# Performance work log

Hardware: AMD Instinct MI355X
Metric: run time of the kernel (lower is better)

The kernel has to match this reference:

```python
import jax, jax.numpy as jnp
import numpy as np

B, S, D = 8, 1024, 1024
H, DH = 16, 64  # num_attention_heads, attention_head_size; H*DH == D


def setup_inputs() -> dict:
    key = jax.random.key(0)
    ks = jax.random.split(key, 6)
    scale = 0.02
    return {
        "hidden_states": jax.random.normal(ks[0], (B, S, D), jnp.float32),
        "right_hidden_states": jax.random.normal(ks[1], (B, S, D), jnp.float32),
        "attention_mask": jnp.ones((B, S, S), jnp.float32),
        "Wq": jax.random.normal(ks[2], (D, H * DH), jnp.float32) * scale,
        "bq": jnp.zeros((H * DH,), jnp.float32),
        "Wk": jax.random.normal(ks[3], (D, H * DH), jnp.float32) * scale,
        "bk": jnp.zeros((H * DH,), jnp.float32),
        "Wv": jax.random.normal(ks[4], (D, H * DH), jnp.float32) * scale,
        "bv": jnp.zeros((H * DH,), jnp.float32),
    }


def _split_heads(x, b):
    # (B, S, H*DH) -> (B, H, S, DH)
    return x.reshape(b, -1, H, DH).transpose(0, 2, 1, 3)


def reference(hidden_states, right_hidden_states, attention_mask, Wq, bq, Wk, bk, Wv, bv):
    b = hidden_states.shape[0]
    q = _split_heads(hidden_states @ Wq + bq, b)          # (B,H,Sq,DH)
    k = _split_heads(right_hidden_states @ Wk + bk, b)    # (B,H,Sk,DH)
    v = _split_heads(right_hidden_states @ Wv + bv, b)    # (B,H,Sk,DH)

    scores = jnp.einsum("bhqd,bhkd->bhqk", q, k) / jnp.sqrt(jnp.asarray(DH, q.dtype))
    scores = jnp.sum(scores, axis=1, keepdims=True)       # (B,1,Sq,Sk) head-summed

    ext = (1.0 - attention_mask[:, None, :, :].astype(scores.dtype)) * -1e9
    probs = jax.nn.softmax(scores + ext, axis=-1)         # (B,1,Sq,Sk)

    ctx = jnp.matmul(probs, v)                            # broadcast -> (B,H,Sq,DH)
    # Faithful to original: reshape WITHOUT transposing heads back.
    return ctx.reshape(b, -1, H * DH)                     # (B,Sq,H*DH)
```

## Files before the change

### kernel.cpp

```cpp
#include <hip/hip_runtime.h>
#include <stdint.h>

constexpr int S = 1024;
constexpr int D = 1024;
constexpr int NB = 8;

typedef __bf16 bf16x8 __attribute__((ext_vector_type(8)));
typedef float floatx4 __attribute__((ext_vector_type(4)));

#define AS1 __attribute__((address_space(1)))
#define AS3 __attribute__((address_space(3)))

__device__ __forceinline__ unsigned short f2bf(float f) {
  unsigned u = __builtin_bit_cast(unsigned, f);
  u += 0x7fffu + ((u >> 16) & 1u);
  return (unsigned short)(u >> 16);
}

__device__ __forceinline__ void gload16(const void* g, void* l) {
  __builtin_amdgcn_global_load_lds((const AS1 unsigned int*)g, (AS3 unsigned int*)l, 16, 0, 0);
}

__global__ __launch_bounds__(256) void prep_kernel(const float4* __restrict__ hs4,
                                                   const float4* __restrict__ rhs4,
                                                   ushort4* __restrict__ hsb4,
                                                   ushort4* __restrict__ rhsb4, int n4,
                                                   const float* __restrict__ Wq,
                                                   const float* __restrict__ Wk,
                                                   const float* __restrict__ Wv,
                                                   unsigned short* __restrict__ Wcat) {
  __shared__ float tile[32][33];
  const int bid = blockIdx.x;
  if (bid < 16384) {
    int i = bid * 256 + threadIdx.x;
    const float4* src;
    ushort4* dst;
    int j;
    if (i < n4) {
      src = hs4; dst = hsb4; j = i;
    } else {
      src = rhs4; dst = rhsb4; j = i - n4;
    }
    float4 v = src[j];
    ushort4 o;
    o.x = f2bf(v.x); o.y = f2bf(v.y); o.z = f2bf(v.z); o.w = f2bf(v.w);
    dst[j] = o;
  } else {
    const int t = bid - 16384;
    const int z = t >> 10;
    const int r = t & 1023;
    const float* W = (z == 0) ? Wq : (z == 1) ? Wk : Wv;
    unsigned short* Wt = Wcat + (long long)z * D * D;
    const int bx = (r & 31) * 32;
    const int by = (r >> 5) * 32;
    const int x = threadIdx.x & 31;
    const int y0 = threadIdx.x >> 5;
    for (int i = 0; i < 4; ++i) {
      int y = y0 + i * 8;
      tile[y][x] = W[(by + y) * D + bx + x];
    }
    __syncthreads();
    for (int i = 0; i < 4; ++i) {
      int y = y0 + i * 8;
      Wt[(long long)(bx + y) * D + by + x] = f2bf(tile[x][y]);
    }
  }
}


#define GEMM_STAGE_SETUP(Abase, lda_, Bbase, ldb_)                            \
  const int srow = tid >> 2;                                                  \
  const int scg = (((tid & 3) ^ ((srow >> 1) & 3)) * 8);                      \
  const unsigned short* aG0 = (Abase) + (long long)srow * (lda_) + scg;       \
  const unsigned short* aG1 = aG0 + (long long)64 * (lda_);                   \
  const unsigned short* bG0 = (Bbase) + (long long)srow * (ldb_) + scg;       \
  const unsigned short* bG1 = bG0 + (long long)64 * (ldb_);                   \
  unsigned short* aL0 = As + w * 512;                                         \
  unsigned short* aL1 = As + w * 512 + 2048;                                  \
  unsigned short* bL0 = Bs + w * 512;                                         \
  unsigned short* bL1 = Bs + w * 512 + 2048;

#define GEMM_KLOOP(Klen)                                                               \
  for (int k0 = 0; k0 < (Klen); k0 += 32) {                                            \
    gload16(aG0 + k0, aL0);                                                            \
    gload16(aG1 + k0, aL1);                                                            \
    gload16(bG0 + k0, bL0);                                                            \
    gload16(bG1 + k0, bL1);                                                            \
    __syncthreads();                                                                   \
    bf16x8 af[4], bfr[4];                                                              \
    for (int t = 0; t < 4; ++t) {                                                      \
      af[t] = *reinterpret_cast<const bf16x8*>(As + (wm + t * 16 + r15) * 32 + pq);    \
      bfr[t] = *reinterpret_cast<const bf16x8*>(Bs + (wn + t * 16 + r15) * 32 + pq);   \
    }                                                                                  \
    for (int mt = 0; mt < 4; ++mt)                                                     \
      for (int nt = 0; nt < 4; ++nt)                                                   \
        acc[mt][nt] =                                                                  \
            __builtin_amdgcn_mfma_f32_16x16x32_bf16(af[mt], bfr[nt], acc[mt][nt], 0, 0, 0); \
    __syncthreads();                                                                   \
  }

#define GEMM_COMMON_IDX                  \
  const int tid = threadIdx.x;           \
  const int lane = tid & 63;             \
  const int w = tid >> 6;                \
  const int r15 = lane & 15;             \
  const int quad = lane >> 4;            \
  const int pq = (quad ^ ((r15 >> 1) & 3)) * 8; \
  const int wm = (w >> 1) * 64;          \
  const int wn = (w & 1) * 64;

#define GEMM_ACC_INIT                    \
  floatx4 acc[4][4];                     \
  for (int i = 0; i < 4; ++i)            \
    for (int j = 0; j < 4; ++j) acc[i][j] = {0.f, 0.f, 0.f, 0.f};

__global__ __launch_bounds__(256, 3) void gemm_qkv_kernel(
    const unsigned short* __restrict__ hsb, const unsigned short* __restrict__ rhsb,
    const unsigned short* __restrict__ Wcat, unsigned short* __restrict__ Qm,
    unsigned short* __restrict__ Km, unsigned short* __restrict__ Vmt,
    const float* __restrict__ bq, const float* __restrict__ bk, const float* __restrict__ bv) {
  __shared__ __align__(16) unsigned short As[128 * 32];
  __shared__ __align__(16) unsigned short Bs[128 * 32];
  GEMM_COMMON_IDX
  const long long n0g = (long long)blockIdx.x * 128;
  const int seg = (int)(n0g >> 10);
  const long long m0 = (long long)blockIdx.y * 128;
  const unsigned short* A = ((seg == 0) ? hsb : rhsb) + m0 * D;
  const unsigned short* Bt = Wcat + n0g * D;
  const float* bias = (seg == 0) ? bq : (seg == 1) ? bk : bv;

  GEMM_STAGE_SETUP(A, D, Bt, D)
  GEMM_ACC_INIT
  GEMM_KLOOP(D)

  const long long nloc0 = n0g & 1023;
  for (int mt = 0; mt < 4; ++mt) {
    for (int nt = 0; nt < 4; ++nt) {
      const long long mrow = m0 + wm + mt * 16 + quad * 4;
      const long long nc = nloc0 + wn + nt * 16 + r15;
      const float bval = bias[nc];
      floatx4 v = acc[mt][nt];
      for (int e = 0; e < 4; ++e) {
        float val = v[e] + bval;
        long long m = mrow + e;
        if (seg == 0) {
          Qm[m * D + nc] = f2bf(val);
        } else if (seg == 1) {
          Km[m * D + nc] = f2bf(val);
        } else {
          Vmt[(m >> 10) * (long long)(S * D) + nc * S + (m & 1023)] = f2bf(val);
        }
      }
    }
  }
}

__global__ __launch_bounds__(256, 3) void gemm_scores_kernel(
    const unsigned short* __restrict__ Qm, const unsigned short* __restrict__ Km,
    const float* __restrict__ mask, unsigned short* __restrict__ E,
    float* __restrict__ rowsumP) {
  __shared__ __align__(16) unsigned short As[128 * 32];
  __shared__ __align__(16) unsigned short Bs[128 * 32];
  GEMM_COMMON_IDX
  const int bid = blockIdx.x;
  const int z = bid & 7;
  const int r = bid >> 3;
  const int by = r >> 3;
  const int bx = r & 7;
  const long long m0 = (long long)by * 128;
  const long long n0 = (long long)bx * 128;
  const unsigned short* A = Qm + (long long)z * S * D + m0 * D;
  const unsigned short* Bt = Km + (long long)z * S * D + n0 * D;

  GEMM_STAGE_SETUP(A, D, Bt, D)
  GEMM_ACC_INIT
  GEMM_KLOOP(D)

  const long long zE = (long long)z * S * 1024;
  float rowpart[4][4];
  for (int mt = 0; mt < 4; ++mt)
    for (int e = 0; e < 4; ++e) rowpart[mt][e] = 0.f;

  for (int mt = 0; mt < 4; ++mt) {
    for (int nt = 0; nt < 4; ++nt) {
      const long long mrow = m0 + wm + mt * 16 + quad * 4;
      const long long nc = n0 + wn + nt * 16 + r15;
      floatx4 v = acc[mt][nt];
      for (int e = 0; e < 4; ++e) {
        long long m = mrow + e;
        float mval = mask[zE + m * 1024 + nc];
        float sc = v[e] * 0.125f + (1.0f - mval) * -1e9f;
        float Ev = __expf(sc);
        E[zE + m * 1024 + nc] = f2bf(Ev);
        rowpart[mt][e] += Ev;
      }
    }
  }
  const int slot = (bx << 11) + ((wn >> 6) << 10);
  for (int mt = 0; mt < 4; ++mt) {
    for (int e = 0; e < 4; ++e) {
      float s = rowpart[mt][e];
      s += __shfl_xor(s, 1, 64);
      s += __shfl_xor(s, 2, 64);
      s += __shfl_xor(s, 4, 64);
      s += __shfl_xor(s, 8, 64);
      if (r15 == 0) {
        int mloc = (int)(m0 + wm + mt * 16 + quad * 4 + e);
        rowsumP[(z << 14) + slot + mloc] = s;
      }
    }
  }
}

__global__ __launch_bounds__(256, 3) void gemm_ctx_kernel(const unsigned short* __restrict__ E,
                                                          const unsigned short* __restrict__ Vmt,
                                                          const float* __restrict__ rowsumP,
                                                          float* __restrict__ out) {
  __shared__ __align__(16) unsigned short As[128 * 32];
  __shared__ __align__(16) unsigned short Bs[128 * 32];
  __shared__ float rsinv[128];
  GEMM_COMMON_IDX
  const int bid = blockIdx.x;
  const int z = bid & 7;
  const int r = bid >> 3;
  const int by = r >> 3;
  const int bx = r & 7;
  const long long m0 = (long long)by * 128;
  const long long n0 = (long long)bx * 128;
  const unsigned short* A = E + (long long)z * S * 1024 + m0 * 1024;
  const unsigned short* Bt = Vmt + (long long)z * S * D + n0 * D;

  if (tid < 128) {
    float s = 0.f;
    for (int t = 0; t < 16; ++t) s += rowsumP[(z << 14) + (t << 10) + (int)m0 + tid];
    rsinv[tid] = 1.0f / s;
  }

  GEMM_STAGE_SETUP(A, 1024, Bt, D)
  GEMM_ACC_INIT
  GEMM_KLOOP(1024)

  for (int mt = 0; mt < 4; ++mt) {
    for (int nt = 0; nt < 4; ++nt) {
      const int r0 = wm + mt * 16 + quad * 4;
      const long long ncol = n0 + wn + nt * 16 + r15;
      floatx4 v = acc[mt][nt];
      for (int e = 0; e < 4; ++e) {
        long long m = m0 + r0 + e;
        float val = v[e] * rsinv[r0 + e];
        out[(long long)z * S * D + (ncol >> 6) * (long long)(S * 64) + m * 64 + (ncol & 63)] =
            val;
      }
    }
  }
}

extern "C" void kernel_launch(void* const* d_in, const int* in_sizes, int n_in, void* d_out,
                              int out_size, void* d_ws, size_t ws_size, hipStream_t stream) {
  const float* hs = (const float*)d_in[0];
  const float* rhs = (const float*)d_in[1];
  const float* mask = (const float*)d_in[2];
  const float* Wq = (const float*)d_in[3];
  const float* bq = (const float*)d_in[4];
  const float* Wk = (const float*)d_in[5];
  const float* bk = (const float*)d_in[6];
  const float* Wv = (const float*)d_in[7];
  const float* bv = (const float*)d_in[8];
  float* out = (float*)d_out;
  char* ws = (char*)d_ws;
  const size_t MB = 1ull << 20;
  unsigned short* Wcat = (unsigned short*)(ws + 0 * MB);
  unsigned short* hsb = (unsigned short*)(ws + 6 * MB);
  unsigned short* rhsb = (unsigned short*)(ws + 22 * MB);
  unsigned short* Qm = (unsigned short*)(ws + 38 * MB);
  unsigned short* Km = (unsigned short*)(ws + 54 * MB);
  unsigned short* Vmt = (unsigned short*)(ws + 70 * MB);
  unsigned short* E = (unsigned short*)(ws + 6 * MB);
  float* rowsumP = (float*)(ws + 22 * MB);

  const int n4 = NB * S * D / 4;
  prep_kernel<<<16384 + 3072, 256, 0, stream>>>((const float4*)hs, (const float4*)rhs,
                                                (ushort4*)hsb, (ushort4*)rhsb, n4, Wq, Wk, Wv,
                                                Wcat);

  gemm_qkv_kernel<<<dim3(24, 64), 256, 0, stream>>>(hsb, rhsb, Wcat, Qm, Km, Vmt, bq, bk, bv);

  gemm_scores_kernel<<<dim3(512), 256, 0, stream>>>(Qm, Km, mask, E, rowsumP);

  gemm_ctx_kernel<<<dim3(512), 256, 0, stream>>>(E, Vmt, rowsumP, out);
}
```

Baseline: 295.0 us.

## Fold Wq·Wkᵀ into a single weight so the K projection GEMM is skipped

Head-summed scores equal hs·Wq·Wkᵀ·rhsᵀ plus bias terms. The change precomputes M = Wq·Wkᵀ/8 with a split-K GEMM, computes the bias cross terms as per-row vectors, then runs one GEMM hs·M and uses rhs directly as the key operand. This drops the separate Q and K projection GEMMs, leaving about two-thirds of the projection work. In exchange it adds a 1024³ weight-product GEMM and a cast pass, it skips the bias matvec when the bias vector is all zero, and it changes bf16 rounding because the precision of the product weight differs.

Result: slower. 309.7 us (+5.0%).

```diff
diff --git a/kernel.cpp b/kernel.cpp
--- a/kernel.cpp
+++ b/kernel.cpp
@@ -17,18 +17,22 @@
   return (unsigned short)(u >> 16);
 }
 
+__device__ __forceinline__ float bf2f(unsigned short x) {
+  unsigned u = ((unsigned)x) << 16;
+  return __builtin_bit_cast(float, u);
+}
+
 __device__ __forceinline__ void gload16(const void* g, void* l) {
   __builtin_amdgcn_global_load_lds((const AS1 unsigned int*)g, (AS3 unsigned int*)l, 16, 0, 0);
 }
 
-__global__ __launch_bounds__(256) void prep_kernel(const float4* __restrict__ hs4,
-                                                   const float4* __restrict__ rhs4,
-                                                   ushort4* __restrict__ hsb4,
-                                                   ushort4* __restrict__ rhsb4, int n4,
-                                                   const float* __restrict__ Wq,
-                                                   const float* __restrict__ Wk,
-                                                   const float* __restrict__ Wv,
-                                                   unsigned short* __restrict__ Wcat) {
+__global__ __launch_bounds__(256) void prep_kernel(
+    const float4* __restrict__ hs4, const float4* __restrict__ rhs4,
+    ushort4* __restrict__ hsb4, ushort4* __restrict__ rhsb4, int n4,
+    const float* __restrict__ Wq, const float* __restrict__ Wk, const float* __restrict__ Wv,
+    unsigned short* __restrict__ WvT, ushort4* __restrict__ Wqb4, ushort4* __restrict__ Wkb4,
+    const float* __restrict__ bq, const float* __restrict__ bk, float* __restrict__ u,
+    float* __restrict__ v, float* __restrict__ cbuf) {
   __shared__ float tile[32][33];
   const int bid = blockIdx.x;
   if (bid < 16384) {
@@ -41,29 +45,58 @@
     } else {
       src = rhs4; dst = rhsb4; j = i - n4;
     }
-    float4 v = src[j];
+    float4 w = src[j];
     ushort4 o;
-    o.x = f2bf(v.x); o.y = f2bf(v.y); o.z = f2bf(v.z); o.w = f2bf(v.w);
+    o.x = f2bf(w.x); o.y = f2bf(w.y); o.z = f2bf(w.z); o.w = f2bf(w.w);
     dst[j] = o;
-  } else {
-    const int t = bid - 16384;
-    const int z = t >> 10;
-    const int r = t & 1023;
-    const float* W = (z == 0) ? Wq : (z == 1) ? Wk : Wv;
-    unsigned short* Wt = Wcat + (long long)z * D * D;
+  } else if (bid < 18432) {
+    int j = (bid - 16384) * 256 + threadIdx.x;
+    const float4* src = (j < 262144) ? (const float4*)Wq : (const float4*)Wk;
+    ushort4* dst = (j < 262144) ? Wqb4 : Wkb4;
+    int jj = (j < 262144) ? j : j - 262144;
+    float4 w = src[jj];
+    ushort4 o;
+    o.x = f2bf(w.x); o.y = f2bf(w.y); o.z = f2bf(w.z); o.w = f2bf(w.w);
+    dst[jj] = o;
+  } else if (bid < 19456) {
+    const int r = bid - 18432;
     const int bx = (r & 31) * 32;
     const int by = (r >> 5) * 32;
     const int x = threadIdx.x & 31;
     const int y0 = threadIdx.x >> 5;
     for (int i = 0; i < 4; ++i) {
       int y = y0 + i * 8;
-      tile[y][x] = W[(by + y) * D + bx + x];
+      tile[y][x] = Wv[(by + y) * D + bx + x];
     }
     __syncthreads();
     for (int i = 0; i < 4; ++i) {
       int y = y0 + i * 8;
-      Wt[(long long)(bx + y) * D + by + x] = f2bf(tile[x][y]);
-    }
+      WvT[(long long)(bx + y) * D + by + x] = f2bf(tile[x][y]);
+    }
+  } else if (bid < 19460) {
+    const int d = (bid - 19456) * 256 + threadIdx.x;
+    const float* row = Wq + (long long)d * 1024;
+    float s = 0.f;
+    for (int c = 0; c < 1024; ++c) s += row[c] * bk[c];
+    u[d] = 0.125f * s;
+  } else if (bid < 19464) {
+    const int d = (bid - 19460) * 256 + threadIdx.x;
+    const float* row = Wk + (long long)d * 1024;
+    float s = 0.f;
+    for (int c = 0; c < 1024; ++c) s += row[c] * bq[c];
+    v[d] = 0.125f * s;
+  } else {
+    __shared__ float sh[256];
+    const int tid = threadIdx.x;
+    float s = 0.f;
+    for (int c = tid; c < 1024; c += 256) s += bq[c] * bk[c];
+    sh[tid] = s;
+    __syncthreads();
+    for (int o = 128; o; o >>= 1) {
+      if (tid < o) sh[tid] += sh[tid + o];
+      __syncthreads();
+    }
+    if (tid == 0) cbuf[0] = 0.125f * sh[0];
   }
 }
 
@@ -114,51 +147,119 @@
   for (int i = 0; i < 4; ++i)            \
     for (int j = 0; j < 4; ++j) acc[i][j] = {0.f, 0.f, 0.f, 0.f};
 
-__global__ __launch_bounds__(256, 3) void gemm_qkv_kernel(
+__global__ __launch_bounds__(256) void wprod_kernel(
+    const unsigned short* __restrict__ Wkb, const unsigned short* __restrict__ Wqb,
+    float* __restrict__ Mtf, const unsigned short* __restrict__ hsb,
+    const unsigned short* __restrict__ rhsb, const float* __restrict__ u,
+    const float* __restrict__ v, const float* __restrict__ cbuf, float* __restrict__ t2,
+    float* __restrict__ t3) {
+  __shared__ __align__(16) unsigned short As[128 * 32];
+  __shared__ __align__(16) unsigned short Bs[128 * 32];
+  const int bid = blockIdx.x;
+  if (bid < 256) {
+    GEMM_COMMON_IDX
+    const int tilei = bid & 63;
+    const int kc = bid >> 6;
+    const int bx = tilei & 7;
+    const int by = tilei >> 3;
+    const unsigned short* A = Wkb + (long long)by * 128 * D + kc * 256;
+    const unsigned short* Bt = Wqb + (long long)bx * 128 * D + kc * 256;
+    GEMM_STAGE_SETUP(A, D, Bt, D)
+    GEMM_ACC_INIT
+    GEMM_KLOOP(256)
+    float* dst = Mtf + ((long long)kc << 20);
+    for (int mt = 0; mt < 4; ++mt)
+      for (int nt = 0; nt < 4; ++nt) {
+        const int mrow = by * 128 + wm + mt * 16 + quad * 4;
+        const int nc = bx * 128 + wn + nt * 16 + r15;
+        floatx4 vv = acc[mt][nt];
+        for (int e = 0; e < 4; ++e) dst[(long long)(mrow + e) * 1024 + nc] = vv[e] * 0.125f;
+      }
+  } else {
+    const int tid = threadIdx.x;
+    const bool isT2 = bid < 288;
+    const int row = (isT2 ? (bid - 256) : (bid - 288)) * 256 + tid;
+    const float* vec = isT2 ? u : v;
+    const unsigned short* mat = isT2 ? hsb : rhsb;
+    float* out = isT2 ? t2 : t3;
+    __shared__ int nz;
+    if (tid == 0) nz = 0;
+    __syncthreads();
+    const float4* u4 = (const float4*)vec;
+    float4 uu = u4[tid];
+    if (uu.x != 0.f || uu.y != 0.f || uu.z != 0.f || uu.w != 0.f) nz = 1;
+    __syncthreads();
+    const float c2 = 0.5f * cbuf[0];
+    if (!nz) {
+      out[row] = c2;
+      return;
+    }
+    const ushort4* r4 = (const ushort4*)(mat + (long long)row * 1024);
+    float s = 0.f;
+    for (int c4 = 0; c4 < 256; ++c4) {
+      ushort4 h = r4[c4];
+      s += bf2f(h.x) * vec[c4 * 4 + 0] + bf2f(h.y) * vec[c4 * 4 + 1] +
+           bf2f(h.z) * vec[c4 * 4 + 2] + bf2f(h.w) * vec[c4 * 4 + 3];
+    }
+    out[row] = s + c2;
+  }
+}
+
+__global__ __launch_bounds__(256) void castM_kernel(const float4* __restrict__ Mtf4,
+                                                    ushort4* __restrict__ Mtb4) {
+  const int j = blockIdx.x * 256 + threadIdx.x;
+  float4 a = Mtf4[j];
+  float4 b = Mtf4[j + 262144];
+  float4 c = Mtf4[j + 524288];
+  float4 d = Mtf4[j + 786432];
+  ushort4 o;
+  o.x = f2bf(a.x + b.x + c.x + d.x);
+  o.y = f2bf(a.y + b.y + c.y + d.y);
+  o.z = f2bf(a.z + b.z + c.z + d.z);
+  o.w = f2bf(a.w + b.w + c.w + d.w);
+  Mtb4[j] = o;
+}
+
+__global__ __launch_bounds__(256) void gemm_fused_kernel(
     const unsigned short* __restrict__ hsb, const unsigned short* __restrict__ rhsb,
-    const unsigned short* __restrict__ Wcat, unsigned short* __restrict__ Qm,
-    unsigned short* __restrict__ Km, unsigned short* __restrict__ Vmt,
-    const float* __restrict__ bq, const float* __restrict__ bk, const float* __restrict__ bv) {
+    const unsigned short* __restrict__ Mtb, const unsigned short* __restrict__ WvT,
+    const float* __restrict__ bv, unsigned short* __restrict__ hsMb,
+    unsigned short* __restrict__ Vmt) {
   __shared__ __align__(16) unsigned short As[128 * 32];
   __shared__ __align__(16) unsigned short Bs[128 * 32];
   GEMM_COMMON_IDX
-  const long long n0g = (long long)blockIdx.x * 128;
-  const int seg = (int)(n0g >> 10);
+  const int seg = (int)(blockIdx.x >> 3);
+  const long long nloc = (blockIdx.x & 7) * 128;
   const long long m0 = (long long)blockIdx.y * 128;
   const unsigned short* A = ((seg == 0) ? hsb : rhsb) + m0 * D;
-  const unsigned short* Bt = Wcat + n0g * D;
-  const float* bias = (seg == 0) ? bq : (seg == 1) ? bk : bv;
+  const unsigned short* Bt = ((seg == 0) ? Mtb : WvT) + nloc * D;
 
   GEMM_STAGE_SETUP(A, D, Bt, D)
   GEMM_ACC_INIT
   GEMM_KLOOP(D)
 
-  const long long nloc0 = n0g & 1023;
   for (int mt = 0; mt < 4; ++mt) {
     for (int nt = 0; nt < 4; ++nt) {
       const long long mrow = m0 + wm + mt * 16 + quad * 4;
-      const long long nc = nloc0 + wn + nt * 16 + r15;
-      const float bval = bias[nc];
-      floatx4 v = acc[mt][nt];
-      for (int e = 0; e < 4; ++e) {
-        float val = v[e] + bval;
-        long long m = mrow + e;
-        if (seg == 0) {
-          Qm[m * D + nc] = f2bf(val);
-        } else if (seg == 1) {
-          Km[m * D + nc] = f2bf(val);
-        } else {
-          Vmt[(m >> 10) * (long long)(S * D) + nc * S + (m & 1023)] = f2bf(val);
+      const long long nc = nloc + wn + nt * 16 + r15;
+      floatx4 vv = acc[mt][nt];
+      if (seg == 0) {
+        for (int e = 0; e < 4; ++e) hsMb[(mrow + e) * D + nc] = f2bf(vv[e]);
+      } else {
+        const float bval = bv[nc];
+        for (int e = 0; e < 4; ++e) {
+          long long m = mrow + e;
+          Vmt[(m >> 10) * (long long)(S * D) + nc * S + (m & 1023)] = f2bf(vv[e] + bval);
         }
       }
     }
   }
 }
 
-__global__ __launch_bounds__(256, 3) void gemm_scores_kernel(
-    const unsigned short* __restrict__ Qm, const unsigned short* __restrict__ Km,
-    const float* __restrict__ mask, unsigned short* __restrict__ E,
-    float* __restrict__ rowsumP) {
+__global__ __launch_bounds__(256) void gemm_scores_kernel(
+    const unsigned short* __restrict__ hsMb, const unsigned short* __restrict__ rhsb,
+    const float* __restrict__ mask, unsigned short* __restrict__ E, float* __restrict__ rowsumP,
+    const float* __restrict__ t2, const float* __restrict__ t3) {
   __shared__ __align__(16) unsigned short As[128 * 32];
   __shared__ __align__(16) unsigned short Bs[128 * 32];
   GEMM_COMMON_IDX
@@ -169,8 +270,8 @@
   const int bx = r & 7;
   const long long m0 = (long long)by * 128;
   const long long n0 = (long long)bx * 128;
-  const unsigned short* A = Qm + (long long)z * S * D + m0 * D;
-  const unsigned short* Bt = Km + (long long)z * S * D + n0 * D;
+  const unsigned short* A = hsMb + (long long)z * S * D + m0 * D;
+  const unsigned short* Bt = rhsb + (long long)z * S * D + n0 * D;
 
   GEMM_STAGE_SETUP(A, D, Bt, D)
   GEMM_ACC_INIT
@@ -185,11 +286,12 @@
     for (int nt = 0; nt < 4; ++nt) {
       const long long mrow = m0 + wm + mt * 16 + quad * 4;
       const long long nc = n0 + wn + nt * 16 + r15;
-      floatx4 v = acc[mt][nt];
+      const float t3v = t3[z * 1024 + nc];
+      floatx4 vv = acc[mt][nt];
       for (int e = 0; e < 4; ++e) {
         long long m = mrow + e;
         float mval = mask[zE + m * 1024 + nc];
-        float sc = v[e] * 0.125f + (1.0f - mval) * -1e9f;
+        float sc = vv[e] + t2[z * 1024 + m] + t3v + (1.0f - mval) * -1e9f;
         float Ev = __expf(sc);
         E[zE + m * 1024 + nc] = f2bf(Ev);
         rowpart[mt][e] += Ev;
@@ -212,10 +314,10 @@
   }
 }
 
-__global__ __launch_bounds__(256, 3) void gemm_ctx_kernel(const unsigned short* __restrict__ E,
-                                                          const unsigned short* __restrict__ Vmt,
-                                                          const float* __restrict__ rowsumP,
-                                                          float* __restrict__ out) {
+__global__ __launch_bounds__(256) void gemm_ctx_kernel(const unsigned short* __restrict__ E,
+                                                       const unsigned short* __restrict__ Vmt,
+                                                       const float* __restrict__ rowsumP,
+                                                       float* __restrict__ out) {
   __shared__ __align__(16) unsigned short As[128 * 32];
   __shared__ __align__(16) unsigned short Bs[128 * 32];
   __shared__ float rsinv[128];
@@ -244,10 +346,10 @@
     for (int nt = 0; nt < 4; ++nt) {
       const int r0 = wm + mt * 16 + quad * 4;
       const long long ncol = n0 + wn + nt * 16 + r15;
-      floatx4 v = acc[mt][nt];
+      floatx4 vv = acc[mt][nt];
       for (int e = 0; e < 4; ++e) {
         long long m = m0 + r0 + e;
-        float val = v[e] * rsinv[r0 + e];
+        float val = vv[e] * rsinv[r0 + e];
         out[(long long)z * S * D + (ncol >> 6) * (long long)(S * 64) + m * 64 + (ncol & 63)] =
             val;
       }
@@ -269,23 +371,34 @@
   float* out = (float*)d_out;
   char* ws = (char*)d_ws;
   const size_t MB = 1ull << 20;
-  unsigned short* Wcat = (unsigned short*)(ws + 0 * MB);
-  unsigned short* hsb = (unsigned short*)(ws + 6 * MB);
-  unsigned short* rhsb = (unsigned short*)(ws + 22 * MB);
-  unsigned short* Qm = (unsigned short*)(ws + 38 * MB);
-  unsigned short* Km = (unsigned short*)(ws + 54 * MB);
-  unsigned short* Vmt = (unsigned short*)(ws + 70 * MB);
-  unsigned short* E = (unsigned short*)(ws + 6 * MB);
-  float* rowsumP = (float*)(ws + 22 * MB);
+  unsigned short* WvT = (unsigned short*)(ws + 0 * MB);
+  unsigned short* Wqb = (unsigned short*)(ws + 2 * MB);
+  unsigned short* Wkb = (unsigned short*)(ws + 4 * MB);
+  unsigned short* Mtb = (unsigned short*)(ws + 6 * MB);
+  float* u = (float*)(ws + 8 * MB);
+  float* v = (float*)(ws + 8 * MB + 4096);
+  float* cbuf = (float*)(ws + 8 * MB + 8192);
+  float* t2 = (float*)(ws + 8 * MB + 16384);
+  float* t3 = (float*)(ws + 8 * MB + 49152);
+  float* rowsumP = (float*)(ws + 8 * MB + 131072);
+  unsigned short* hsb = (unsigned short*)(ws + 9 * MB);
+  unsigned short* rhsb = (unsigned short*)(ws + 25 * MB);
+  unsigned short* hsMb = (unsigned short*)(ws + 41 * MB);
+  float* Mtf = (float*)(ws + 41 * MB);
+  unsigned short* Vmt = (unsigned short*)(ws + 57 * MB);
+  unsigned short* E = (unsigned short*)(ws + 9 * MB);
 
   const int n4 = NB * S * D / 4;
-  prep_kernel<<<16384 + 3072, 256, 0, stream>>>((const float4*)hs, (const float4*)rhs,
-                                                (ushort4*)hsb, (ushort4*)rhsb, n4, Wq, Wk, Wv,
-                                                Wcat);
-
-  gemm_qkv_kernel<<<dim3(24, 64), 256, 0, stream>>>(hsb, rhsb, Wcat, Qm, Km, Vmt, bq, bk, bv);
-
-  gemm_scores_kernel<<<dim3(512), 256, 0, stream>>>(Qm, Km, mask, E, rowsumP);
-
-  gemm_ctx_kernel<<<dim3(512), 256, 0, stream>>>(E, Vmt, rowsumP, out);
-}
+  prep_kernel<<<19465, 256, 0, stream>>>((const float4*)hs, (const float4*)rhs, (ushort4*)hsb,
+                                         (ushort4*)rhsb, n4, Wq, Wk, Wv, WvT, (ushort4*)Wqb,
+                                         (ushort4*)Wkb, bq, bk, u, v, cbuf);
+
+  wprod_kernel<<<320, 256, 0, stream>>>(Wkb, Wqb, Mtf, hsb, rhsb, u, v, cbuf, t2, t3);
+  castM_kernel<<<1024, 256, 0, stream>>>((const float4*)Mtf, (ushort4*)Mtb);
+
+  gemm_fused_kernel<<<dim3(16, 64), 256, 0, stream>>>(hsb, rhsb, Mtb, WvT, bv, hsMb, Vmt);
+
+  gemm_scores_kernel<<<512, 256, 0, stream>>>(hsMb, rhsb, mask, E, rowsumP, t2, t3);
+
+  gemm_ctx_kernel<<<512, 256, 0, stream>>>(E, Vmt, rowsumP, out);
+}
```
